# Kernel optimization log

Hardware: AMD Instinct MI355X
Metric: run time of the kernel (lower is better)

Reference implementation:

```python
import jax, jax.numpy as jnp
import numpy as np

N_NODES = 100000   # n_nodes in data_config
K = 32             # edge_threshold (neighbors per node)
D = 64             # in_channel == out_channel == emb_size, heads = 1
B = 1024           # index batch size
NEG_SLOPE = 0.2


def setup_inputs() -> dict:
    key = jax.random.key(0)
    ks = jax.random.split(key, 10)
    glorot = (6.0 / (D + D)) ** 0.5
    all_embed = jax.random.normal(ks[0], (N_NODES, D), jnp.float32) * 0.1     # xavier-ish
    W = jax.random.uniform(ks[1], (D, D), jnp.float32, -glorot, glorot)       # GATConv.weight (heads*out = 64)
    g_att = (6.0 / (1 + 2 * D)) ** 0.5
    att = jax.random.uniform(ks[2], (1, 1, 2 * D), jnp.float32, -g_att, g_att)  # GATConv.att
    bias = jnp.zeros((D,), jnp.float32)                                       # GATConv.bias (zeros init)
    edges_matrix = jax.random.randint(ks[3], (N_NODES, K), 0, N_NODES)
    user = jax.random.randint(ks[4], (B,), 0, 10000)
    pos_item = jax.random.randint(ks[5], (B,), 0, N_NODES)
    neg_item = jax.random.randint(ks[6], (B,), 0, N_NODES)
    pos_rules = jax.random.randint(ks[7], (B,), 0, N_NODES)
    selected_neg_outfits_rules = jax.random.randint(ks[8], (B,), 0, N_NODES)
    return {
        "all_embed": all_embed, "W": W, "att": att, "bias": bias,
        "user": user, "pos_item": pos_item, "neg_item": neg_item,
        "edges_matrix": edges_matrix, "pos_rules": pos_rules,
        "selected_neg_outfits_rules": selected_neg_outfits_rules,
    }


def reference(all_embed, W, att, bias, user, pos_item, neg_item,
              edges_matrix, pos_rules, selected_neg_outfits_rules):
    n, d = all_embed.shape
    k = edges_matrix.shape[1]

    # build_edge: src = repeated node index, dst = neighbor index; then edges.t()
    # -> edge_index[0] = source j, edge_index[1] = target i (PyG source_to_target)
    src = jnp.repeat(jnp.arange(n), k)          # [N*K]
    dst = edges_matrix.reshape(-1)              # [N*K]
    valid = src != dst                          # remove_self_loops (mask, static shape)
    loop = jnp.arange(n)                        # add_self_loops
    src = jnp.concatenate([src, loop])          # [E], E = N*K + N
    dst = jnp.concatenate([dst, loop])
    valid = jnp.concatenate([valid, jnp.ones((n,), bool)])

    # x = mm(x, W).view(-1, heads=1, out=64)
    h = all_embed @ W                           # [N, D]

    # alpha = sum(cat([x_i, x_j], -1) * att, -1); precontract att with h (cheap)
    a_i = att[0, 0, :d]                         # target half
    a_j = att[0, 0, d:]                         # source half
    s_i = h @ a_i                               # [N]
    s_j = h @ a_j                               # [N]
    alpha = s_i[dst] + s_j[src]                 # [E]
    alpha = jnp.where(alpha >= 0, alpha, NEG_SLOPE * alpha)  # leaky_relu
    alpha = jnp.where(valid, alpha, -1e9)       # removed self-loop edges drop out of softmax

    # segment softmax over target nodes (every node has a self loop -> no empty segment)
    m = jax.lax.stop_gradient(jax.ops.segment_max(alpha, dst, num_segments=n))
    e = jnp.exp(alpha - m[dst])
    denom = jax.ops.segment_sum(e, dst, num_segments=n)
    a = e / (denom[dst] + 1e-16)                # [E]

    # message = x_j * alpha ; aggregate = scatter-add at targets
    out = jax.ops.segment_sum(h[src] * a[:, None], dst, num_segments=n)  # [N, D]

    # update: mean over heads (1 head -> identity) + bias
    out = out + bias

    # GraphConv_KGAT: dropout (identity in eval) then F.normalize (L2, eps=1e-12)
    norm = jnp.linalg.norm(out, axis=-1, keepdims=True)
    gcn_embedding = out / jnp.maximum(norm, 1e-12)
    return gcn_embedding
```

## Files before the change

kernel.cpp:

```cpp
#include <hip/hip_runtime.h>
#include <hip/hip_bf16.h>

#define NEG_SLOPE 0.2f
#define BSHIFT 8
#define BSIZE  (1 << BSHIFT)
#define CAP    9216
#define NBMAX  400
#define SRC_MASK 0x1FFFF

__device__ __forceinline__ float lrelu(float x) { return fmaxf(x, NEG_SLOPE * x); }
__device__ __forceinline__ float bf2f(unsigned short u) {
    return __uint_as_float((unsigned)u << 16);
}
__device__ __forceinline__ unsigned short f2bf(float f) {
    unsigned u = __float_as_uint(f);
    return (unsigned short)((u + 0x7fffu + ((u >> 16) & 1u)) >> 16);
}

__global__ __launch_bounds__(256, 4) void k_gemm(
    const float* __restrict__ A, const float* __restrict__ W,
    const float* __restrict__ att,
    unsigned short* __restrict__ h16, float* __restrict__ s_i, float* __restrict__ s_j, int n)
{
    __shared__ float At[64 * 68];
    __shared__ float Wl[64 * 68];
    const int tid  = threadIdx.x;
    const int lane = tid & 63;
    const int tx = tid & 15, ty = tid >> 4;
    const int r0 = ty * 4, c0 = tx * 4;
    const long row0 = (long)blockIdx.x * 64;

    {
        int r = tid & 63;
        int kb = (tid >> 6) * 4;
        long gr = row0 + r; if (gr >= n) gr = n - 1;
        const float4* Ar = (const float4*)(A + gr * 64);
#pragma unroll
        for (int p = 0; p < 4; ++p) {
            int k0 = p * 16 + kb;
            float4 a = Ar[k0 >> 2];
            At[(k0 + 0) * 68 + r] = a.x;
            At[(k0 + 1) * 68 + r] = a.y;
            At[(k0 + 2) * 68 + r] = a.z;
            At[(k0 + 3) * 68 + r] = a.w;
        }
        int c = (tid & 15) * 4;
        int rr = tid >> 4;
#pragma unroll
        for (int p = 0; p < 4; ++p) {
            int k = rr + p * 16;
            *(float4*)&Wl[k * 68 + c] = *(const float4*)(W + k * 64 + c);
        }
    }
    __syncthreads();

    float acc[4][4] = {};
#pragma unroll 4
    for (int k = 0; k < 64; ++k) {
        float4 a = *(const float4*)&At[k * 68 + r0];
        float4 w = *(const float4*)&Wl[k * 68 + c0];
        acc[0][0] = fmaf(a.x, w.x, acc[0][0]);
        acc[0][1] = fmaf(a.x, w.y, acc[0][1]);
        acc[0][2] = fmaf(a.x, w.z, acc[0][2]);
        acc[0][3] = fmaf(a.x, w.w, acc[0][3]);
        acc[1][0] = fmaf(a.y, w.x, acc[1][0]);
        acc[1][1] = fmaf(a.y, w.y, acc[1][1]);
        acc[1][2] = fmaf(a.y, w.z, acc[1][2]);
        acc[1][3] = fmaf(a.y, w.w, acc[1][3]);
        acc[2][0] = fmaf(a.z, w.x, acc[2][0]);
        acc[2][1] = fmaf(a.z, w.y, acc[2][1]);
        acc[2][2] = fmaf(a.z, w.z, acc[2][2]);
        acc[2][3] = fmaf(a.z, w.w, acc[2][3]);
        acc[3][0] = fmaf(a.w, w.x, acc[3][0]);
        acc[3][1] = fmaf(a.w, w.y, acc[3][1]);
        acc[3][2] = fmaf(a.w, w.z, acc[3][2]);
        acc[3][3] = fmaf(a.w, w.w, acc[3][3]);
    }

    const int rowlim = (int)(((long)n - row0) < 64 ? (n - row0) : 64);

#pragma unroll
    for (int i = 0; i < 4; ++i) {
        int r = r0 + i;
        if (r < rowlim) {
            uint2 uv;
            uv.x = (unsigned)f2bf(acc[i][0]) | ((unsigned)f2bf(acc[i][1]) << 16);
            uv.y = (unsigned)f2bf(acc[i][2]) | ((unsigned)f2bf(acc[i][3]) << 16);
            *(uint2*)(h16 + (row0 + r) * 64 + c0) = uv;
        }
    }

    float4 avi = *(const float4*)(att + c0);
    float4 avj = *(const float4*)(att + 64 + c0);
#pragma unroll
    for (int i = 0; i < 4; ++i) {
        float pi = acc[i][0] * avi.x;
        pi = fmaf(acc[i][1], avi.y, pi);
        pi = fmaf(acc[i][2], avi.z, pi);
        pi = fmaf(acc[i][3], avi.w, pi);
        float pj = acc[i][0] * avj.x;
        pj = fmaf(acc[i][1], avj.y, pj);
        pj = fmaf(acc[i][2], avj.z, pj);
        pj = fmaf(acc[i][3], avj.w, pj);
#pragma unroll
        for (int o = 1; o <= 8; o <<= 1) {
            pi += __shfl_xor(pi, o, 64);
            pj += __shfl_xor(pj, o, 64);
        }
        int r = r0 + i;
        if ((lane & 15) == 0 && r < rowlim) {
            s_i[row0 + r] = pi;
            s_j[row0 + r] = pj;
        }
    }
}

__global__ __launch_bounds__(256) void k_binA(
    const int* __restrict__ edges, int* __restrict__ bcursor,
    unsigned* __restrict__ pairs, int n_edges, int nb)
{
    __shared__ int hist[NBMAX];
    __shared__ int cur[NBMAX];
    int t = threadIdx.x;
    for (int b = t; b < nb; b += 256) hist[b] = 0;
    __syncthreads();
    long base = (long)blockIdx.x * 8192;

    for (int k = 0; k < 32; ++k) {
        long e = base + k * 256 + t;
        if (e < n_edges) {
            int d = edges[e];
            int i = (int)(e >> 5);
            if (d != i) atomicAdd(&hist[d >> BSHIFT], 1);
        }
    }
    __syncthreads();

    for (int b = t; b < nb; b += 256) {
        int c = hist[b];
        int g = 0;
        if (c) g = atomicAdd(&bcursor[b], c);
        cur[b] = b * CAP + g;
    }
    __syncthreads();

    for (int k = 0; k < 32; ++k) {
        long e = base + k * 256 + t;
        if (e < n_edges) {
            int d = edges[e];
            int i = (int)(e >> 5);
            if (d != i) {
                int b = d >> BSHIFT;
                int slot = atomicAdd(&cur[b], 1);
                if (slot < (b + 1) * CAP)
                    pairs[slot] = ((unsigned)(d & (BSIZE - 1)) << 17) | (unsigned)i;
            }
        }
    }
}

__global__ __launch_bounds__(512) void k_binB(
    const int* __restrict__ bcursor, unsigned* __restrict__ pairs,
    int* __restrict__ offs, int* __restrict__ counts, int n)
{
    __shared__ unsigned pl[CAP];
    __shared__ unsigned srt[CAP];
    __shared__ int hist[BSIZE];
    __shared__ int scn[BSIZE];
    __shared__ int cur[BSIZE];
    int b = blockIdx.x, t = threadIdx.x;
    int cnt = bcursor[b];
    if (cnt > CAP) cnt = CAP;
    long wb = (long)b * CAP;

    for (int s = t; s < cnt; s += 512) pl[s] = pairs[wb + s];
    if (t < BSIZE) hist[t] = 0;
    __syncthreads();
    for (int s = t; s < cnt; s += 512) atomicAdd(&hist[pl[s] >> 17], 1);
    __syncthreads();

    if (t < BSIZE) scn[t] = hist[t];
    __syncthreads();
    for (int d = 1; d < BSIZE; d <<= 1) {
        int v = (t >= d && t < BSIZE) ? scn[t - d] : 0;
        __syncthreads();
        if (t < BSIZE) scn[t] += v;
        __syncthreads();
    }
    if (t < BSIZE) {
        int start = scn[t] - hist[t];
        int dg = (b << BSHIFT) + t;
        if (dg < n) {
            offs[dg] = (int)(wb + start);
            counts[dg] = hist[t];
        }
        cur[t] = start;
    }
    __syncthreads();

    for (int s = t; s < cnt; s += 512) {
        unsigned pk = pl[s];
        int pos = atomicAdd(&cur[pk >> 17], 1);
        srt[pos] = pk & SRC_MASK;
    }
    __syncthreads();

    for (int s = t; s < cnt; s += 512)
        ((int*)pairs)[wb + s] = (int)srt[s];
}

__global__ __launch_bounds__(256) void k_gather(
    const int* __restrict__ offs, const int* __restrict__ counts,
    const int* __restrict__ srcl, const unsigned short* __restrict__ h16,
    const float* __restrict__ s_i, const float* __restrict__ s_j,
    const float* __restrict__ bias, float* __restrict__ out, int n)
{
    int gw = (blockIdx.x * 256 + threadIdx.x) >> 6;
    int lane = threadIdx.x & 63;
    if (gw >= n) return;
    const int d = gw;
    const int off = offs[d], deg = counts[d];
    const float si = s_i[d];
    const float es = __expf(lrelu(si + s_j[d]));

    const int g  = lane >> 3;
    const int li = lane & 7;
    const char* hb = (const char*)h16 + (li << 4);

    float acc[8];
#pragma unroll
    for (int i = 0; i < 8; ++i) acc[i] = 0.f;
    float denp = 0.f;

    for (int base = 0; base < deg; base += 64) {
        int t = base + lane;
        int cnt = min(64, deg - base);
        int soff = 0; float w = 0.f;
        if (t < deg) {
            int s = srcl[off + t];
            soff = s << 7;
            w = __expf(lrelu(si + s_j[s]));
        }
        denp += w;
        for (int j = 0; j < cnt; j += 16) {
            int i0 = j + g, i1 = j + 8 + g;
            float w0 = __shfl(w, i0, 64);
            int   o0 = __shfl(soff, i0, 64);
            float w1 = __shfl(w, i1, 64);
            int   o1 = __shfl(soff, i1, 64);
            uint4 ha = *(const uint4*)(hb + o0);
            uint4 hc = *(const uint4*)(hb + o1);
            acc[0] = fmaf(__uint_as_float(ha.x << 16),          w0, acc[0]);
            acc[1] = fmaf(__uint_as_float(ha.x & 0xffff0000u),  w0, acc[1]);
            acc[2] = fmaf(__uint_as_float(ha.y << 16),          w0, acc[2]);
            acc[3] = fmaf(__uint_as_float(ha.y & 0xffff0000u),  w0, acc[3]);
            acc[4] = fmaf(__uint_as_float(ha.z << 16),          w0, acc[4]);
            acc[5] = fmaf(__uint_as_float(ha.z & 0xffff0000u),  w0, acc[5]);
            acc[6] = fmaf(__uint_as_float(ha.w << 16),          w0, acc[6]);
            acc[7] = fmaf(__uint_as_float(ha.w & 0xffff0000u),  w0, acc[7]);
            acc[0] = fmaf(__uint_as_float(hc.x << 16),          w1, acc[0]);
            acc[1] = fmaf(__uint_as_float(hc.x & 0xffff0000u),  w1, acc[1]);
            acc[2] = fmaf(__uint_as_float(hc.y << 16),          w1, acc[2]);
            acc[3] = fmaf(__uint_as_float(hc.y & 0xffff0000u),  w1, acc[3]);
            acc[4] = fmaf(__uint_as_float(hc.z << 16),          w1, acc[4]);
            acc[5] = fmaf(__uint_as_float(hc.z & 0xffff0000u),  w1, acc[5]);
            acc[6] = fmaf(__uint_as_float(hc.w << 16),          w1, acc[6]);
            acc[7] = fmaf(__uint_as_float(hc.w & 0xffff0000u),  w1, acc[7]);
        }
    }

#pragma unroll
    for (int o = 8; o <= 32; o <<= 1) {
#pragma unroll
        for (int i = 0; i < 8; ++i)
            acc[i] += __shfl_xor(acc[i], o, 64);
    }
#pragma unroll
    for (int o = 32; o; o >>= 1) denp += __shfl_xor(denp, o, 64);

    uint4 hd = *(const uint4*)(hb + (d << 7));
    float den = denp + es + 1e-16f;
    float rden = 1.f / den;
    const float4* pb = (const float4*)(bias + (li << 3));
    float4 b0 = pb[0], b1 = pb[1];

    float v[8];
    v[0] = fmaf(__uint_as_float(hd.x << 16),         es, acc[0]) * rden + b0.x;
    v[1] = fmaf(__uint_as_float(hd.x & 0xffff0000u), es, acc[1]) * rden + b0.y;
    v[2] = fmaf(__uint_as_float(hd.y << 16),         es, acc[2]) * rden + b0.z;
    v[3] = fmaf(__uint_as_float(hd.y & 0xffff0000u), es, acc[3]) * rden + b0.w;
    v[4] = fmaf(__uint_as_float(hd.z << 16),         es, acc[4]) * rden + b1.x;
    v[5] = fmaf(__uint_as_float(hd.z & 0xffff0000u), es, acc[5]) * rden + b1.y;
    v[6] = fmaf(__uint_as_float(hd.w << 16),         es, acc[6]) * rden + b1.z;
    v[7] = fmaf(__uint_as_float(hd.w & 0xffff0000u), es, acc[7]) * rden + b1.w;

    float sq = 0.f;
#pragma unroll
    for (int i = 0; i < 8; ++i) sq = fmaf(v[i], v[i], sq);
#pragma unroll
    for (int o = 1; o <= 4; o <<= 1) sq += __shfl_xor(sq, o, 64);
    float rn = 1.f / fmaxf(sqrtf(sq), 1e-12f);

    if (g < 2) {
        float4 ov;
        if (g == 0) ov = make_float4(v[0] * rn, v[1] * rn, v[2] * rn, v[3] * rn);
        else        ov = make_float4(v[4] * rn, v[5] * rn, v[6] * rn, v[7] * rn);
        *(float4*)(out + ((long)d << 6) + (li << 3) + (g << 2)) = ov;
    }
}

extern "C" void kernel_launch(void* const* d_in, const int* in_sizes, int n_in,
                              void* d_out, int out_size, void* d_ws, size_t ws_size,
                              hipStream_t stream)
{
    const float* A    = (const float*)d_in[0];
    const float* W    = (const float*)d_in[1];
    const float* att  = (const float*)d_in[2];
    const float* bias = (const float*)d_in[3];
    const int* edges  = (const int*)d_in[7];

    int n = in_sizes[0] / 64;
    int n_edges = in_sizes[7];
    int nb = (n + BSIZE - 1) >> BSHIFT;

    unsigned short* h16 = (unsigned short*)d_ws;
    float* s_i      = (float*)(h16 + (long)n * 64);
    float* s_j      = s_i + n;
    int* offs       = (int*)(s_j + n);
    int* counts     = offs + n;
    int* bcursor    = counts + n;
    unsigned* pairs = (unsigned*)(bcursor + 512);

    (void)hipMemsetAsync(bcursor, 0, 512 * sizeof(int), stream);

    int blocks_rows = (n + 63) / 64;
    k_gemm<<<blocks_rows, 256, 0, stream>>>(A, W, att, h16, s_i, s_j, n);

    int blocks_binA = (n_edges + 8191) / 8192;
    k_binA<<<blocks_binA, 256, 0, stream>>>(edges, bcursor, pairs, n_edges, nb);

    k_binB<<<nb, 512, 0, stream>>>(bcursor, pairs, offs, counts, n);

    int blocks_waves = ((long)n * 64 + 255) / 256;
    k_gather<<<blocks_waves, 256, 0, stream>>>(offs, counts, (const int*)pairs, h16,
                                               s_i, s_j, bias, (float*)d_out, n);
}
```

Before: 223.6 us.

## Replace two-level bucket sort with global atomic count, scan, and scatter CSR build

The two-pass bucketed binning (shared-memory histogram per 256-node bucket, then per-bucket LDS sort) is replaced by a classic CSR build: global atomic degree count, two-kernel prefix scan, and an atomic-cursor scatter of source indices. This removes the fixed CAP bucket capacity and the large LDS sort kernel but relies on global atomics per edge (3.2M) on random destinations, twice, plus more kernel launches. Neighbor order within each destination becomes nondeterministic, which changes float summation order in the gather.

New measurement: 595.9 us. 2.67x slower.

```diff
diff --git a/kernel.cpp b/kernel.cpp
--- a/kernel.cpp
+++ b/kernel.cpp
@@ -2,11 +2,6 @@
 #include <hip/hip_bf16.h>
 
 #define NEG_SLOPE 0.2f
-#define BSHIFT 8
-#define BSIZE  (1 << BSHIFT)
-#define CAP    9216
-#define NBMAX  400
-#define SRC_MASK 0x1FFFF
 
 __device__ __forceinline__ float lrelu(float x) { return fmaxf(x, NEG_SLOPE * x); }
 __device__ __forceinline__ float bf2f(unsigned short u) {
@@ -115,98 +110,86 @@
     }
 }
 
-__global__ __launch_bounds__(256) void k_binA(
-    const int* __restrict__ edges, int* __restrict__ bcursor,
-    unsigned* __restrict__ pairs, int n_edges, int nb)
-{
-    __shared__ int hist[NBMAX];
-    __shared__ int cur[NBMAX];
-    int t = threadIdx.x;
-    for (int b = t; b < nb; b += 256) hist[b] = 0;
-    __syncthreads();
-    long base = (long)blockIdx.x * 8192;
-
-    for (int k = 0; k < 32; ++k) {
-        long e = base + k * 256 + t;
+__global__ __launch_bounds__(256) void k_count(
+    const int* __restrict__ edges, int* __restrict__ counts, int n_edges)
+{
+    long base = (long)blockIdx.x * 2048 + threadIdx.x;
+#pragma unroll
+    for (int k = 0; k < 8; ++k) {
+        long e = base + k * 256;
         if (e < n_edges) {
             int d = edges[e];
             int i = (int)(e >> 5);
-            if (d != i) atomicAdd(&hist[d >> BSHIFT], 1);
-        }
-    }
-    __syncthreads();
-
-    for (int b = t; b < nb; b += 256) {
-        int c = hist[b];
-        int g = 0;
-        if (c) g = atomicAdd(&bcursor[b], c);
-        cur[b] = b * CAP + g;
-    }
-    __syncthreads();
-
-    for (int k = 0; k < 32; ++k) {
-        long e = base + k * 256 + t;
+            if (d != i) atomicAdd(&counts[d], 1);
+        }
+    }
+}
+
+__global__ __launch_bounds__(1024) void k_scanA(
+    const int* __restrict__ counts, int* __restrict__ bsum, int n)
+{
+    __shared__ int sc[1024];
+    int t = threadIdx.x;
+    long idx = (long)blockIdx.x * 1024 + t;
+    sc[t] = (idx < n) ? counts[idx] : 0;
+    __syncthreads();
+    for (int s = 512; s > 0; s >>= 1) {
+        if (t < s) sc[t] += sc[t + s];
+        __syncthreads();
+    }
+    if (t == 0) bsum[blockIdx.x] = sc[0];
+}
+
+__global__ __launch_bounds__(1024) void k_scan(
+    const int* __restrict__ counts, const int* __restrict__ bsum,
+    int* __restrict__ offs, int* __restrict__ cursor, int n)
+{
+    __shared__ int sc[1024];
+    int t = threadIdx.x, b = blockIdx.x;
+
+    sc[t] = (t < b) ? bsum[t] : 0;
+    __syncthreads();
+    for (int s = 512; s > 0; s >>= 1) {
+        if (t < s) sc[t] += sc[t + s];
+        __syncthreads();
+    }
+    int base = sc[0];
+    __syncthreads();
+
+    long idx = (long)b * 1024 + t;
+    int c = (idx < n) ? counts[idx] : 0;
+    sc[t] = c;
+    __syncthreads();
+    for (int d = 1; d < 1024; d <<= 1) {
+        int v = (t >= d) ? sc[t - d] : 0;
+        __syncthreads();
+        sc[t] += v;
+        __syncthreads();
+    }
+    if (idx < n) {
+        int excl = sc[t] - c + base;
+        offs[idx] = excl;
+        cursor[idx] = excl;
+    }
+}
+
+__global__ __launch_bounds__(256) void k_scatter(
+    const int* __restrict__ edges, int* __restrict__ cursor,
+    int* __restrict__ srcl, int n_edges)
+{
+    long base = (long)blockIdx.x * 2048 + threadIdx.x;
+#pragma unroll
+    for (int k = 0; k < 8; ++k) {
+        long e = base + k * 256;
         if (e < n_edges) {
             int d = edges[e];
             int i = (int)(e >> 5);
             if (d != i) {
-                int b = d >> BSHIFT;
-                int slot = atomicAdd(&cur[b], 1);
-                if (slot < (b + 1) * CAP)
-                    pairs[slot] = ((unsigned)(d & (BSIZE - 1)) << 17) | (unsigned)i;
+                int pos = atomicAdd(&cursor[d], 1);
+                srcl[pos] = i;
             }
         }
     }
-}
-
-__global__ __launch_bounds__(512) void k_binB(
-    const int* __restrict__ bcursor, unsigned* __restrict__ pairs,
-    int* __restrict__ offs, int* __restrict__ counts, int n)
-{
-    __shared__ unsigned pl[CAP];
-    __shared__ unsigned srt[CAP];
-    __shared__ int hist[BSIZE];
-    __shared__ int scn[BSIZE];
-    __shared__ int cur[BSIZE];
-    int b = blockIdx.x, t = threadIdx.x;
-    int cnt = bcursor[b];
-    if (cnt > CAP) cnt = CAP;
-    long wb = (long)b * CAP;
-
-    for (int s = t; s < cnt; s += 512) pl[s] = pairs[wb + s];
-    if (t < BSIZE) hist[t] = 0;
-    __syncthreads();
-    for (int s = t; s < cnt; s += 512) atomicAdd(&hist[pl[s] >> 17], 1);
-    __syncthreads();
-
-    if (t < BSIZE) scn[t] = hist[t];
-    __syncthreads();
-    for (int d = 1; d < BSIZE; d <<= 1) {
-        int v = (t >= d && t < BSIZE) ? scn[t - d] : 0;
-        __syncthreads();
-        if (t < BSIZE) scn[t] += v;
-        __syncthreads();
-    }
-    if (t < BSIZE) {
-        int start = scn[t] - hist[t];
-        int dg = (b << BSHIFT) + t;
-        if (dg < n) {
-            offs[dg] = (int)(wb + start);
-            counts[dg] = hist[t];
-        }
-        cur[t] = start;
-    }
-    __syncthreads();
-
-    for (int s = t; s < cnt; s += 512) {
-        unsigned pk = pl[s];
-        int pos = atomicAdd(&cur[pk >> 17], 1);
-        srt[pos] = pk & SRC_MASK;
-    }
-    __syncthreads();
-
-    for (int s = t; s < cnt; s += 512)
-        ((int*)pairs)[wb + s] = (int)srt[s];
 }
 
 __global__ __launch_bounds__(256) void k_gather(
@@ -321,27 +304,29 @@
 
     int n = in_sizes[0] / 64;
     int n_edges = in_sizes[7];
-    int nb = (n + BSIZE - 1) >> BSHIFT;
+    int nchunks = (n + 1023) / 1024;
 
     unsigned short* h16 = (unsigned short*)d_ws;
-    float* s_i      = (float*)(h16 + (long)n * 64);
-    float* s_j      = s_i + n;
-    int* offs       = (int*)(s_j + n);
-    int* counts     = offs + n;
-    int* bcursor    = counts + n;
-    unsigned* pairs = (unsigned*)(bcursor + 512);
-
-    (void)hipMemsetAsync(bcursor, 0, 512 * sizeof(int), stream);
+    float* s_i    = (float*)(h16 + (long)n * 64);
+    float* s_j    = s_i + n;
+    int* offs     = (int*)(s_j + n);
+    int* counts   = offs + n;
+    int* cursor   = counts + n;
+    int* bsum     = cursor + n;
+    int* srcl     = bsum + 128;
+
+    (void)hipMemsetAsync(counts, 0, (size_t)n * sizeof(int), stream);
 
     int blocks_rows = (n + 63) / 64;
     k_gemm<<<blocks_rows, 256, 0, stream>>>(A, W, att, h16, s_i, s_j, n);
 
-    int blocks_binA = (n_edges + 8191) / 8192;
-    k_binA<<<blocks_binA, 256, 0, stream>>>(edges, bcursor, pairs, n_edges, nb);
-
-    k_binB<<<nb, 512, 0, stream>>>(bcursor, pairs, offs, counts, n);
+    int blocks_e = (n_edges + 2047) / 2048;
+    k_count<<<blocks_e, 256, 0, stream>>>(edges, counts, n_edges);
+    k_scanA<<<nchunks, 1024, 0, stream>>>(counts, bsum, n);
+    k_scan<<<nchunks, 1024, 0, stream>>>(counts, bsum, offs, cursor, n);
+    k_scatter<<<blocks_e, 256, 0, stream>>>(edges, cursor, srcl, n_edges);
 
     int blocks_waves = ((long)n * 64 + 255) / 256;
-    k_gather<<<blocks_waves, 256, 0, stream>>>(offs, counts, (const int*)pairs, h16,
+    k_gather<<<blocks_waves, 256, 0, stream>>>(offs, counts, srcl, h16,
                                                s_i, s_j, bias, (float*)d_out, n);
 }
```

## Replace atomic counting sort in bin kernel with stable ballot-based LSD radix sort

Applied to the files above, without the earlier changes.

The per-bucket sort in k_binB no longer builds a histogram with shared atomics and scatters by atomic cursors. It now runs an 8-pass stable binary radix sort over the destination bits, using wavefront ballots and popcounts plus a block-wide prefix scan for each pass. Segment offsets are then recovered by boundary detection. This gives a deterministic, stable order (sources stay sorted within each destination) and removes atomic contention, but it costs eight passes with many syncthreads and scans, which may be slower than the single atomic pass.

Result: slower. 272.9 us (+22.1%).

```diff
diff --git a/kernel.cpp b/kernel.cpp
--- a/kernel.cpp
+++ b/kernel.cpp
@@ -163,50 +163,85 @@
     const int* __restrict__ bcursor, unsigned* __restrict__ pairs,
     int* __restrict__ offs, int* __restrict__ counts, int n)
 {
-    __shared__ unsigned pl[CAP];
-    __shared__ unsigned srt[CAP];
-    __shared__ int hist[BSIZE];
-    __shared__ int scn[BSIZE];
-    __shared__ int cur[BSIZE];
-    int b = blockIdx.x, t = threadIdx.x;
-    int cnt = bcursor[b];
-    if (cnt > CAP) cnt = CAP;
-    long wb = (long)b * CAP;
-
-    for (int s = t; s < cnt; s += 512) pl[s] = pairs[wb + s];
-    if (t < BSIZE) hist[t] = 0;
-    __syncthreads();
-    for (int s = t; s < cnt; s += 512) atomicAdd(&hist[pl[s] >> 17], 1);
-    __syncthreads();
-
-    if (t < BSIZE) scn[t] = hist[t];
-    __syncthreads();
-    for (int d = 1; d < BSIZE; d <<= 1) {
-        int v = (t >= d && t < BSIZE) ? scn[t - d] : 0;
+    __shared__ unsigned bb[2][CAP];
+    __shared__ int sseg[2][256];
+    __shared__ int offl[257];
+    const int b = blockIdx.x, t = threadIdx.x;
+    const int w = t >> 6, lane = t & 63;
+    int cnt = bcursor[b]; if (cnt > CAP) cnt = CAP;
+    const long wb = (long)b * CAP;
+    const int nch = (cnt + 511) >> 9;
+    const unsigned long long below = ((unsigned long long)1 << lane) - 1ull;
+
+    for (int i = t; i < cnt; i += 512) bb[0][i] = pairs[wb + i];
+    __syncthreads();
+
+    int p = 0;
+    for (int pass = 0; pass < 8; ++pass) {
+        const int bit = 17 + pass;
+        if (t < 256) sseg[0][t] = 0;
         __syncthreads();
-        if (t < BSIZE) scn[t] += v;
+        for (int c = 0; c < nch; ++c) {
+            int i = (c << 9) + t;
+            bool valid = (i < cnt);
+            unsigned v = valid ? bb[p][i] : 0u;
+            unsigned long long bal1 = __ballot(valid && ((v >> bit) & 1u));
+            unsigned long long balv = __ballot(valid);
+            int n0 = __popcll(balv) - __popcll(bal1);
+            if (lane == 0) sseg[0][(c << 3) + w] = n0;
+        }
         __syncthreads();
-    }
-    if (t < BSIZE) {
-        int start = scn[t] - hist[t];
-        int dg = (b << BSHIFT) + t;
-        if (dg < n) {
-            offs[dg] = (int)(wb + start);
-            counts[dg] = hist[t];
-        }
-        cur[t] = start;
-    }
-    __syncthreads();
-
-    for (int s = t; s < cnt; s += 512) {
-        unsigned pk = pl[s];
-        int pos = atomicAdd(&cur[pk >> 17], 1);
-        srt[pos] = pk & SRC_MASK;
-    }
-    __syncthreads();
-
-    for (int s = t; s < cnt; s += 512)
-        ((int*)pairs)[wb + s] = (int)srt[s];
+        int ping = 0;
+        for (int d = 1; d < 256; d <<= 1) {
+            if (t < 256) {
+                int vv = sseg[ping][t];
+                if (t >= d) vv += sseg[ping][t - d];
+                sseg[ping ^ 1][t] = vv;
+            }
+            __syncthreads();
+            ping ^= 1;
+        }
+        const int N0 = sseg[ping][255];
+        for (int c = 0; c < nch; ++c) {
+            int i = (c << 9) + t;
+            bool valid = (i < cnt);
+            unsigned v = valid ? bb[p][i] : 0u;
+            int b1 = (int)((v >> bit) & 1u);
+            unsigned long long bal1 = __ballot(valid && b1);
+            unsigned long long balv = __ballot(valid);
+            int seg = (c << 3) + w;
+            int n0seg = __popcll(balv) - __popcll(bal1);
+            int scan0ex = sseg[ping][seg] - n0seg;
+            if (valid) {
+                int dest;
+                if (!b1) {
+                    dest = scan0ex + __popcll((balv & ~bal1) & below);
+                } else {
+                    int pv = seg << 6; if (pv > cnt) pv = cnt;
+                    dest = N0 + (pv - scan0ex) + __popcll(bal1 & below);
+                }
+                bb[p ^ 1][dest] = v;
+            }
+        }
+        __syncthreads();
+        p ^= 1;
+    }
+
+    if (t < 257) offl[t] = cnt;
+    __syncthreads();
+    for (int i = t; i < cnt; i += 512) {
+        int k  = (int)(bb[p][i] >> 17);
+        int kp = (i > 0) ? (int)(bb[p][i - 1] >> 17) : -1;
+        for (int d = kp + 1; d <= k; ++d) offl[d] = i;
+    }
+    __syncthreads();
+    int dg = (b << BSHIFT) + t;
+    if (t < BSIZE && dg < n) {
+        offs[dg]   = (int)(wb + offl[t]);
+        counts[dg] = offl[t + 1] - offl[t];
+    }
+    for (int i = t; i < cnt; i += 512)
+        ((int*)pairs)[wb + i] = (int)(bb[p][i] & SRC_MASK);
 }
 
 __global__ __launch_bounds__(256) void k_gather(
```

## Stage binned edge pairs in shared memory and flush bucket runs contiguously

Applied to the files above, without the earlier changes.

The edge-binning kernel now loads edges into registers once, builds a per-block histogram plus an exclusive scan, and scatters pairs into a shared-memory staging buffer ordered by bucket. Each wave then copies its buckets' contiguous runs to global memory in a coalesced way, replacing scattered global writes and the second read of the edge array. Block size doubles to 512 threads. In exchange the kernel uses about 40KB of shared memory, which may lower occupancy, and it relies on nb being at most 512.

Result: faster. 218.0 us (-2.5%).

```diff
diff --git a/kernel.cpp b/kernel.cpp
--- a/kernel.cpp
+++ b/kernel.cpp
@@ -115,47 +115,75 @@
     }
 }
 
-__global__ __launch_bounds__(256) void k_binA(
+__global__ __launch_bounds__(512) void k_binA(
     const int* __restrict__ edges, int* __restrict__ bcursor,
     unsigned* __restrict__ pairs, int n_edges, int nb)
 {
-    __shared__ int hist[NBMAX];
-    __shared__ int cur[NBMAX];
-    int t = threadIdx.x;
-    for (int b = t; b < nb; b += 256) hist[b] = 0;
-    __syncthreads();
-    long base = (long)blockIdx.x * 8192;
-
-    for (int k = 0; k < 32; ++k) {
-        long e = base + k * 256 + t;
+    __shared__ int hist[512];
+    __shared__ int scn[512];
+    __shared__ int st[512];
+    __shared__ int cur[512];
+    __shared__ int gbase[512];
+    __shared__ unsigned lp[8192];
+    const int t = threadIdx.x;
+    const long base = (long)blockIdx.x * 8192;
+
+    int er[16];
+#pragma unroll
+    for (int k = 0; k < 16; ++k) {
+        long e = base + k * 512 + t;
+        int d = -1;
         if (e < n_edges) {
-            int d = edges[e];
-            int i = (int)(e >> 5);
-            if (d != i) atomicAdd(&hist[d >> BSHIFT], 1);
-        }
-    }
-    __syncthreads();
-
-    for (int b = t; b < nb; b += 256) {
-        int c = hist[b];
-        int g = 0;
-        if (c) g = atomicAdd(&bcursor[b], c);
-        cur[b] = b * CAP + g;
-    }
-    __syncthreads();
-
-    for (int k = 0; k < 32; ++k) {
-        long e = base + k * 256 + t;
-        if (e < n_edges) {
-            int d = edges[e];
-            int i = (int)(e >> 5);
-            if (d != i) {
-                int b = d >> BSHIFT;
-                int slot = atomicAdd(&cur[b], 1);
-                if (slot < (b + 1) * CAP)
-                    pairs[slot] = ((unsigned)(d & (BSIZE - 1)) << 17) | (unsigned)i;
-            }
-        }
+            d = edges[e];
+            if (d == (int)(e >> 5)) d = -1;
+        }
+        er[k] = d;
+    }
+
+    hist[t] = 0;
+    __syncthreads();
+#pragma unroll
+    for (int k = 0; k < 16; ++k)
+        if (er[k] >= 0) atomicAdd(&hist[er[k] >> BSHIFT], 1);
+    __syncthreads();
+
+    scn[t] = hist[t];
+    __syncthreads();
+    for (int d = 1; d < 512; d <<= 1) {
+        int v = (t >= d) ? scn[t - d] : 0;
+        __syncthreads();
+        scn[t] += v;
+        __syncthreads();
+    }
+    int s0 = scn[t] - hist[t];
+    st[t] = s0;
+    cur[t] = s0;
+    gbase[t] = 0;
+    if (t < nb && hist[t] > 0) gbase[t] = atomicAdd(&bcursor[t], hist[t]);
+    __syncthreads();
+
+#pragma unroll
+    for (int k = 0; k < 16; ++k) {
+        int d = er[k];
+        if (d >= 0) {
+            int b = d >> BSHIFT;
+            int slot = atomicAdd(&cur[b], 1);
+            long e = base + k * 512 + t;
+            lp[slot] = ((unsigned)(d & (BSIZE - 1)) << 17) | (unsigned)(e >> 5);
+        }
+    }
+    __syncthreads();
+
+    const int w = t >> 6, lane = t & 63;
+    for (int b = w; b < nb; b += 8) {
+        int cnt = hist[b];
+        int gb  = gbase[b];
+        int cw  = cnt;
+        if (gb + cw > CAP) cw = CAP - gb;
+        long gdst = (long)b * CAP + gb;
+        int sb = st[b];
+        for (int s = lane; s < cw; s += 64)
+            pairs[gdst + s] = lp[sb + s];
     }
 }
 
@@ -337,7 +365,7 @@
     k_gemm<<<blocks_rows, 256, 0, stream>>>(A, W, att, h16, s_i, s_j, n);
 
     int blocks_binA = (n_edges + 8191) / 8192;
-    k_binA<<<blocks_binA, 256, 0, stream>>>(edges, bcursor, pairs, n_edges, nb);
+    k_binA<<<blocks_binA, 512, 0, stream>>>(edges, bcursor, pairs, n_edges, nb);
 
     k_binB<<<nb, 512, 0, stream>>>(bcursor, pairs, offs, counts, n);
 
```
